# Kernel optimization log

Hardware: AMD Instinct MI355X
Metric: run time of the kernel (lower is better)

The kernel has to match this reference:

```python
import jax, jax.numpy as jnp
import numpy as np

D_MODEL = 64
NUM_MODES = 16
SCALE = 1.0 / (D_MODEL * D_MODEL)


def setup_inputs() -> dict:
    key = jax.random.key(0)
    kq, kk, kv = jax.random.split(key, 3)
    shape = (4, 2048, 64, 64)  # (b, t, c, mw_dim)
    q = jax.random.normal(kq, shape, dtype=jnp.float32)
    k = jax.random.normal(kk, shape, dtype=jnp.float32)
    v = jax.random.normal(kv, shape, dtype=jnp.float32)
    return {"q": q, "k": k, "v": v}


def reference(q, k, v):
    b, t, c, mw = q.shape
    modes = min(t // 2, NUM_MODES)
    # permute (b,t,c,mw) -> (b,h,d,t) with h=mw_dim, d=c
    xq = jnp.transpose(q, (0, 3, 2, 1))
    xk = jnp.transpose(k, (0, 3, 2, 1))
    xv = jnp.transpose(v, (0, 3, 2, 1))
    # rfft over time, keep lowest `modes` frequency bins (contiguous low-pass)
    qf = jnp.fft.rfft(xq, axis=-1)[..., :modes]  # (b,h,d,modes) complex64
    kf = jnp.fft.rfft(xk, axis=-1)[..., :modes]
    vf = jnp.fft.rfft(xv, axis=-1)[..., :modes]
    # complex-domain attention over the reduced mode set
    qk = jnp.einsum('bhdx,bhdy->bhxy', qf, kf)  # (b,h,modes,modes)
    qk = jnp.tanh(qk)  # complex tanh, matching torch.tanh on cfloat
    qkv = jnp.einsum('bhxy,bhdy->bhdx', qk, vf)  # (b,h,d,modes)
    # scatter back into full rfft spectrum (zeros elsewhere)
    out_ft = jnp.zeros((b, mw, c, t // 2 + 1), dtype=qkv.dtype)
    out_ft = out_ft.at[..., :modes].set(qkv)
    out = jnp.fft.irfft(out_ft * SCALE, n=t, axis=-1)  # (b,h,d,t) float32
    return jnp.transpose(out, (0, 3, 2, 1))  # (b,t,c,mw)
```

## Files before the change

kernel.cpp:

```cpp
#include <hip/hip_runtime.h>
#include <hip/hip_bf16.h>
#include <math.h>


#define T_DIM 2048
#define DH 4096
#define DH2 2048
#define CH 8
#define TPCH 64
#define NPH 16
#define TT 16

__device__ inline float4 f4add(float4 a, float4 b) {
    return make_float4(a.x + b.x, a.y + b.y, a.z + b.z, a.w + b.w);
}
__device__ inline float4 f4sub(float4 a, float4 b) {
    return make_float4(a.x - b.x, a.y - b.y, a.z - b.z, a.w - b.w);
}

__global__ void init_tables(float* __restrict__ WA, float* __restrict__ Bt2) {
    int i = blockIdx.x * 256 + threadIdx.x;
    const float TWO_PI = 6.2831853071795864769f;
    if (i < 512 * 32) {
        int t = i >> 5, r = i & 31, m = r >> 1;
        int ph = (m * t) & 2047;
        float ang = TWO_PI * (float)ph * (1.0f / 2048.0f);
        WA[i] = (r & 1) ? sinf(ang) : cosf(ang);
    }
    int i2 = i - 512 * 32;
    if (i2 >= 0 && i2 < 1024 * 32) {
        int t = i2 >> 5, r = i2 & 31, m = r >> 1;
        int ph = (m * t) & 2047;
        float ang = TWO_PI * (float)ph * (1.0f / 2048.0f);
        const float S2 = 1.0f / (4096.0f * 2048.0f);
        float coef = (m == 0 ? 1.0f : 2.0f) * S2;
        float val;
        if (!(r & 1)) val = coef * cosf(ang);
        else          val = (m == 0) ? 0.0f : -coef * sinf(ang);
        Bt2[i2] = val;
    }
}


#define LOADP(PH, X0, X1, X2, X3) do {                                         \
    size_t t0 = (size_t)(tbase + (PH) * 4);                                    \
    X0 = src4[t0 * 1024 + f4];                                                 \
    X1 = src4[(t0 + 512) * 1024 + f4];                                         \
    X2 = src4[(t0 + 1024) * 1024 + f4];                                        \
    X3 = src4[(t0 + 1536) * 1024 + f4];                                        \
} while (0)

#define FOLDW(BUF, X0, X1, X2, X3) do {                                        \
    float4 fu0 = f4add(X0, X2), fu1 = f4add(X1, X3);                           \
    float4 fd0 = f4sub(X0, X2), fd1 = f4sub(X1, X3);                           \
    wslab[(BUF) * 256 + 0 * 64 + widx] = f4add(fu0, fu1);                      \
    wslab[(BUF) * 256 + 1 * 64 + widx] = f4sub(fu0, fu1);                      \
    wslab[(BUF) * 256 + 2 * 64 + widx] = fd0;                                  \
    wslab[(BUF) * 256 + 3 * 64 + widx] = fd1;                                  \
} while (0)

#define COMP(BUF, PH) do {                                                     \
    _Pragma("unroll")                                                          \
    for (int i = 0; i < 4; i++) {                                              \
        float ee  = elds[iw][BUF][0][i][lane];                                 \
        float ff  = elds[iw][BUF][1][i][lane];                                 \
        float dd0 = elds[iw][BUF][2][i][lane];                                 \
        float dd1 = elds[iw][BUF][3][i][lane];                                 \
        const float* tw = WA + (size_t)(c * TPCH + (PH) * 4 + i) * 32;         \
        _Pragma("unroll")                                                      \
        for (int m = 0; m < 16; m++) {                                         \
            float cm = tw[2 * m], sm = tw[2 * m + 1];                          \
            if ((m & 3) == 0) {                                                \
                accR[m] = fmaf(cm, ee, accR[m]);                               \
                accI[m] = fmaf(-sm, ee, accI[m]);                              \
            } else if ((m & 3) == 2) {                                         \
                accR[m] = fmaf(cm, ff, accR[m]);                               \
                accI[m] = fmaf(-sm, ff, accI[m]);                              \
            } else if ((m & 3) == 1) {                                         \
                accR[m] = fmaf(cm, dd0, fmaf(-sm, dd1, accR[m]));              \
                accI[m] = fmaf(-sm, dd0, fmaf(-cm, dd1, accI[m]));             \
            } else {                                                           \
                accR[m] = fmaf(cm, dd0, fmaf(sm, dd1, accR[m]));               \
                accI[m] = fmaf(-sm, dd0, fmaf(cm, dd1, accI[m]));              \
            }                                                                  \
        }                                                                      \
    }                                                                          \
} while (0)

__global__ __launch_bounds__(256) void stageA(
        const float* __restrict__ q, const float* __restrict__ k,
        const float* __restrict__ v, const float* __restrict__ WA,
        float* __restrict__ P) {
    __shared__ float elds[4][2][4][4][64];

    int tid  = threadIdx.x;
    int iw   = tid >> 6;
    int lane = tid & 63;
    int li   = lane >> 4;
    int lc   = lane & 15;
    int bx   = blockIdx.x;
    int c    = blockIdx.y;
    int tz   = blockIdx.z;
    int tensor = tz >> 2, b = tz & 3;

    const float* srcf = (tensor == 0 ? q : tensor == 1 ? k : v)
                        + (size_t)b * T_DIM * DH;
    const float4* src4 = (const float4*)srcf;
    const int f4    = bx * 64 + iw * 16 + lc;
    const int tbase = c * TPCH + li;

    float4* wslab = (float4*)&elds[iw][0][0][0][0];
    const int widx = li * 16 + lc;

    float accR[16], accI[16];
    #pragma unroll
    for (int m = 0; m < 16; m++) { accR[m] = 0.f; accI[m] = 0.f; }

    float4 a0, a1, a2, a3, b0, b1, b2, b3;

    LOADP(0, a0, a1, a2, a3);
    FOLDW(0, a0, a1, a2, a3);
    LOADP(1, b0, b1, b2, b3);

    for (int ph = 0; ph < NPH - 2; ph += 2) {
        LOADP(ph + 2, a0, a1, a2, a3);
        COMP(0, ph);
        FOLDW(1, b0, b1, b2, b3);
        LOADP(ph + 3, b0, b1, b2, b3);
        COMP(1, ph + 1);
        FOLDW(0, a0, a1, a2, a3);
    }
    COMP(0, NPH - 2);
    FOLDW(1, b0, b1, b2, b3);
    COMP(1, NPH - 1);

    float* pp = P + ((size_t)(tz * CH + c) * 32) * DH + bx * 256 + tid;
    #pragma unroll
    for (int m = 0; m < 16; m++) {
        pp[(size_t)m * DH]        = accR[m];
        pp[(size_t)(16 + m) * DH] = accI[m];
    }
}

__global__ __launch_bounds__(256) void reduceP(const float4* __restrict__ P,
                                               float4* __restrict__ Y) {
    size_t i   = (size_t)blockIdx.x * 256 + threadIdx.x;
    size_t tzj = i >> 10;
    size_t dh4 = i & 1023;
    size_t tz  = tzj >> 5;
    size_t j   = tzj & 31;
    const float4* p = P + ((tz * CH) * 32 + j) * 1024 + dh4;
    float4 s = make_float4(0.f, 0.f, 0.f, 0.f);
    #pragma unroll
    for (int cc = 0; cc < CH; cc++) {
        float4 t = p[(size_t)cc * 32 * 1024];
        s.x += t.x; s.y += t.y; s.z += t.z; s.w += t.w;
    }
    Y[i] = s;
}

__global__ __launch_bounds__(256) void stageB(const float* __restrict__ Y,
                                              float* __restrict__ G) {
    __shared__ float qf[64 * 33];
    __shared__ float kf[64 * 33];
    __shared__ float vf[64 * 33];
    __shared__ float qkr[16 * 17];
    __shared__ float qki[16 * 17];

    int tid = threadIdx.x;
    int bh  = blockIdx.x;
    int b   = bh >> 6;
    int h   = bh & 63;

    #pragma unroll
    for (int tensor = 0; tensor < 3; tensor++) {
        float* dst = (tensor == 0 ? qf : tensor == 1 ? kf : vf);
        const float* yp = Y + ((size_t)(tensor * 4 + b) * 32) * DH + h;
        #pragma unroll
        for (int it = 0; it < 8; it++) {
            int p = it * 256 + tid;
            int d = p & 63, j = p >> 6;
            dst[d * 33 + j] = yp[(size_t)j * DH + d * 64];
        }
    }
    __syncthreads();

    int x = tid >> 4, y = tid & 15;
    float ar = 0.f, ai = 0.f;
    #pragma unroll 4
    for (int d = 0; d < 64; d++) {
        float qr = qf[d * 33 + x],      qi = qf[d * 33 + 16 + x];
        float kr = kf[d * 33 + y],      ki = kf[d * 33 + 16 + y];
        ar += qr * kr - qi * ki;
        ai += qr * ki + qi * kr;
    }
    float re, im;
    float a2 = 2.f * ar, b2 = 2.f * ai;
    if (fabsf(a2) < 80.f) {
        float den = coshf(a2) + cosf(b2);
        re = sinhf(a2) / den;
        im = sinf(b2) / den;
    } else {
        re = copysignf(1.f, ar);
        im = 0.f;
    }
    qkr[x * 17 + y] = re;
    qki[x * 17 + y] = im;
    __syncthreads();

    int xx = tid & 15, db = tid >> 4;
    #pragma unroll
    for (int i = 0; i < 4; i++) {
        int d = db + i * 16;
        float cr = 0.f, ci = 0.f;
        #pragma unroll
        for (int yy = 0; yy < 16; yy++) {
            float tr = qkr[xx * 17 + yy], ti = qki[xx * 17 + yy];
            float vr = vf[d * 33 + yy],   vi = vf[d * 33 + 16 + yy];
            cr += tr * vr - ti * vi;
            ci += tr * vi + ti * vr;
        }
        G[((size_t)b * 32 + xx) * DH + d * 64 + h]      = cr;
        G[((size_t)b * 32 + 16 + xx) * DH + d * 64 + h] = ci;
    }
}

__global__ __launch_bounds__(256) void stageC(const float* __restrict__ G,
                                              const float* __restrict__ Bt2,
                                              float* __restrict__ out) {
    __shared__ float w[TT * 32];
    int tid = threadIdx.x;
    int c   = blockIdx.y;
    int b   = blockIdx.z;

    #pragma unroll
    for (int it = 0; it < TT * 32 / 256; it++)
        w[it * 256 + tid] = Bt2[c * (TT * 32) + it * 256 + tid];
    __syncthreads();

    int dh2 = blockIdx.x * 256 + tid;
    float2 gr[16], gi[16];
    const float2* gp = (const float2*)G + (size_t)b * 32 * DH2 + dh2;
    #pragma unroll
    for (int m = 0; m < 16; m++) {
        gr[m] = gp[(size_t)m * DH2];
        gi[m] = gp[(size_t)(16 + m) * DH2];
    }

    float2* o0 = (float2*)out + ((size_t)b * T_DIM + (size_t)c * TT) * DH2 + dh2;
    #pragma unroll 2
    for (int tl = 0; tl < TT; tl++) {
        const float* ww = &w[tl * 32];
        float2 E = make_float2(0.f, 0.f), O = make_float2(0.f, 0.f);
        #pragma unroll
        for (int m = 0; m < 16; m += 2) {
            E.x = fmaf(ww[2 * m],     gr[m].x, E.x);
            E.x = fmaf(ww[2 * m + 1], gi[m].x, E.x);
            E.y = fmaf(ww[2 * m],     gr[m].y, E.y);
            E.y = fmaf(ww[2 * m + 1], gi[m].y, E.y);
        }
        #pragma unroll
        for (int m = 1; m < 16; m += 2) {
            O.x = fmaf(ww[2 * m],     gr[m].x, O.x);
            O.x = fmaf(ww[2 * m + 1], gi[m].x, O.x);
            O.y = fmaf(ww[2 * m],     gr[m].y, O.y);
            O.y = fmaf(ww[2 * m + 1], gi[m].y, O.y);
        }
        o0[(size_t)tl * DH2] = make_float2(E.x + O.x, E.y + O.y);
        o0[(size_t)(tl + 1024) * DH2] = make_float2(E.x - O.x, E.y - O.y);
    }
}

extern "C" void kernel_launch(void* const* d_in, const int* in_sizes, int n_in,
                              void* d_out, int out_size, void* d_ws, size_t ws_size,
                              hipStream_t stream) {
    const float* q = (const float*)d_in[0];
    const float* k = (const float*)d_in[1];
    const float* v = (const float*)d_in[2];
    float* out = (float*)d_out;

    char* ws = (char*)d_ws;
    float* WA  = (float*)ws;
    float* Bt2 = (float*)(ws + 65536);
    const size_t base = 65536 + 131072;

    const size_t psz = (size_t)12 * CH * 32 * DH * 4;
    const size_t ysz = 6291456;
    float* P = (float*)(ws + base);
    float* Y = (float*)(ws + base + psz);
    float* G = (float*)(ws + base + psz + ysz);

    init_tables<<<192, 256, 0, stream>>>(WA, Bt2);
    stageA<<<dim3(16, CH, 12), 256, 0, stream>>>(q, k, v, WA, P);
    reduceP<<<1536, 256, 0, stream>>>((const float4*)P, (float4*)Y);
    stageB<<<256, 256, 0, stream>>>(Y, G);
    stageC<<<dim3(8, 64, 4), 256, 0, stream>>>(G, Bt2, out);
}
```

Baseline: 481.1 us.

## Stage input slabs via direct global-to-LDS async loads with double buffering

Replaces the register-staged loads and folded LDS writes in stageA with 16-byte global_load_lds transfers straight into a double-buffered shared tile. The 4-point butterfly fold moves from the loader into the compute step, where each thread reads raw values and folds them itself. Explicit vmcnt waits and barriers order the async copies against compute. This aims to cut VGPR pressure and load-to-store latency, at the cost of more LDS reads per compute step and extra block-wide barriers.

```diff
diff --git a/kernel.cpp b/kernel.cpp
--- a/kernel.cpp
+++ b/kernel.cpp
@@ -10,13 +10,6 @@
 #define TPCH 64
 #define NPH 16
 #define TT 16
-
-__device__ inline float4 f4add(float4 a, float4 b) {
-    return make_float4(a.x + b.x, a.y + b.y, a.z + b.z, a.w + b.w);
-}
-__device__ inline float4 f4sub(float4 a, float4 b) {
-    return make_float4(a.x - b.x, a.y - b.y, a.z - b.z, a.w - b.w);
-}
 
 __global__ void init_tables(float* __restrict__ WA, float* __restrict__ Bt2) {
     int i = blockIdx.x * 256 + threadIdx.x;
@@ -41,31 +34,31 @@
     }
 }
 
-
-#define LOADP(PH, X0, X1, X2, X3) do {                                         \
-    size_t t0 = (size_t)(tbase + (PH) * 4);                                    \
-    X0 = src4[t0 * 1024 + f4];                                                 \
-    X1 = src4[(t0 + 512) * 1024 + f4];                                         \
-    X2 = src4[(t0 + 1024) * 1024 + f4];                                        \
-    X3 = src4[(t0 + 1536) * 1024 + f4];                                        \
-} while (0)
-
-#define FOLDW(BUF, X0, X1, X2, X3) do {                                        \
-    float4 fu0 = f4add(X0, X2), fu1 = f4add(X1, X3);                           \
-    float4 fd0 = f4sub(X0, X2), fd1 = f4sub(X1, X3);                           \
-    wslab[(BUF) * 256 + 0 * 64 + widx] = f4add(fu0, fu1);                      \
-    wslab[(BUF) * 256 + 1 * 64 + widx] = f4sub(fu0, fu1);                      \
-    wslab[(BUF) * 256 + 2 * 64 + widx] = fd0;                                  \
-    wslab[(BUF) * 256 + 3 * 64 + widx] = fd1;                                  \
+__device__ __forceinline__ void async16(const void* gptr, void* lptr) {
+    __builtin_amdgcn_global_load_lds(
+        (const __attribute__((address_space(1))) unsigned int*)gptr,
+        (__attribute__((address_space(3))) unsigned int*)lptr,
+        16, 0, 0);
+}
+
+
+#define STAGE(PH, BUF) do {                                                    \
+    size_t t0 = (size_t)(c * TPCH + (PH) * 4 + iw);                            \
+    async16(&src4[t0 * 1024 + gcol],          &tile[BUF][iw][0][0]);           \
+    async16(&src4[(t0 + 512) * 1024 + gcol],  &tile[BUF][iw][1][0]);           \
+    async16(&src4[(t0 + 1024) * 1024 + gcol], &tile[BUF][iw][2][0]);           \
+    async16(&src4[(t0 + 1536) * 1024 + gcol], &tile[BUF][iw][3][0]);           \
 } while (0)
 
 #define COMP(BUF, PH) do {                                                     \
     _Pragma("unroll")                                                          \
     for (int i = 0; i < 4; i++) {                                              \
-        float ee  = elds[iw][BUF][0][i][lane];                                 \
-        float ff  = elds[iw][BUF][1][i][lane];                                 \
-        float dd0 = elds[iw][BUF][2][i][lane];                                 \
-        float dd1 = elds[iw][BUF][3][i][lane];                                 \
+        const float* tp = (const float*)&tile[BUF][i][0][0];                   \
+        float x0 = tp[tid], x1 = tp[256 + tid];                                \
+        float x2 = tp[512 + tid], x3 = tp[768 + tid];                          \
+        float fu0 = x0 + x2, fu1 = x1 + x3;                                    \
+        float ee  = fu0 + fu1, ff = fu0 - fu1;                                 \
+        float dd0 = x0 - x2, dd1 = x1 - x3;                                    \
         const float* tw = WA + (size_t)(c * TPCH + (PH) * 4 + i) * 32;         \
         _Pragma("unroll")                                                      \
         for (int m = 0; m < 16; m++) {                                         \
@@ -91,13 +84,11 @@
         const float* __restrict__ q, const float* __restrict__ k,
         const float* __restrict__ v, const float* __restrict__ WA,
         float* __restrict__ P) {
-    __shared__ float elds[4][2][4][4][64];
+    __shared__ float4 tile[2][4][4][64];
 
     int tid  = threadIdx.x;
     int iw   = tid >> 6;
     int lane = tid & 63;
-    int li   = lane >> 4;
-    int lc   = lane & 15;
     int bx   = blockIdx.x;
     int c    = blockIdx.y;
     int tz   = blockIdx.z;
@@ -106,33 +97,29 @@
     const float* srcf = (tensor == 0 ? q : tensor == 1 ? k : v)
                         + (size_t)b * T_DIM * DH;
     const float4* src4 = (const float4*)srcf;
-    const int f4    = bx * 64 + iw * 16 + lc;
-    const int tbase = c * TPCH + li;
-
-    float4* wslab = (float4*)&elds[iw][0][0][0][0];
-    const int widx = li * 16 + lc;
+    const int gcol = bx * 64 + lane;
 
     float accR[16], accI[16];
     #pragma unroll
     for (int m = 0; m < 16; m++) { accR[m] = 0.f; accI[m] = 0.f; }
 
-    float4 a0, a1, a2, a3, b0, b1, b2, b3;
-
-    LOADP(0, a0, a1, a2, a3);
-    FOLDW(0, a0, a1, a2, a3);
-    LOADP(1, b0, b1, b2, b3);
-
-    for (int ph = 0; ph < NPH - 2; ph += 2) {
-        LOADP(ph + 2, a0, a1, a2, a3);
+    STAGE(0, 0);
+    STAGE(1, 1);
+
+    for (int ph = 0; ph < NPH; ph += 2) {
+        asm volatile("s_waitcnt vmcnt(4)" ::: "memory");
+        __builtin_amdgcn_s_barrier();
         COMP(0, ph);
-        FOLDW(1, b0, b1, b2, b3);
-        LOADP(ph + 3, b0, b1, b2, b3);
+        __builtin_amdgcn_s_barrier();
+        if (ph + 2 < NPH) STAGE(ph + 2, 0);
+
+        if (ph + 3 < NPH) { asm volatile("s_waitcnt vmcnt(4)" ::: "memory"); }
+        else              { asm volatile("s_waitcnt vmcnt(0)" ::: "memory"); }
+        __builtin_amdgcn_s_barrier();
         COMP(1, ph + 1);
-        FOLDW(0, a0, a1, a2, a3);
-    }
-    COMP(0, NPH - 2);
-    FOLDW(1, b0, b1, b2, b3);
-    COMP(1, NPH - 1);
+        __builtin_amdgcn_s_barrier();
+        if (ph + 3 < NPH) STAGE(ph + 3, 1);
+    }
 
     float* pp = P + ((size_t)(tz * CH + c) * 32) * DH + bx * 256 + tid;
     #pragma unroll
```

New measurement: 469.1 us. -2.5%, faster.
